# Performance work log

Hardware: AMD Instinct MI355X
Metric: run time of the kernel (lower is better)

The kernel has to match this reference:

```python
import jax, jax.numpy as jnp
from jax import lax
import numpy as np

D_MODEL = 512
D_PROJ = 256
PATCH = 4
NL = 8
D_STATE = 16
D_CONV = 4
EXPAND = 2
D_INNER = EXPAND * D_MODEL          # 1024
DT_RANK = (D_MODEL + 15) // 16      # 32
B = 4
SEQ = 1024
NF = 1
EPS = 1e-5


def setup_inputs() -> dict:
    key = jax.random.key(0)
    ks = jax.random.split(key, 12)
    s = 0.02
    def rn(k, shape):
        return jax.random.normal(k, shape, jnp.float32) * s
    A_init = jnp.log(jnp.arange(1, D_STATE + 1, dtype=jnp.float32))  # (n,)
    return {
        "time_series": jax.random.normal(ks[0], (B, SEQ, NF), jnp.float32),
        "mask": jnp.ones((B, SEQ), jnp.int32),
        "emb_w": rn(ks[1], (D_MODEL, PATCH)),
        "emb_b": jnp.zeros((D_MODEL,), jnp.float32),
        "norm_w": jnp.ones((NL, D_MODEL), jnp.float32),
        "in_w": rn(ks[2], (NL, 2, 2 * D_INNER, D_MODEL)),
        "conv_w": rn(ks[3], (NL, 2, D_INNER, D_CONV)),
        "conv_b": jnp.zeros((NL, 2, D_INNER), jnp.float32),
        "xproj_w": rn(ks[4], (NL, 2, DT_RANK + 2 * D_STATE, D_INNER)),
        "dt_w": rn(ks[5], (NL, 2, D_INNER, DT_RANK)),
        "dt_b": jnp.full((NL, 2, D_INNER), float(np.log(np.expm1(0.01))), jnp.float32),
        "A_log": jnp.broadcast_to(A_init, (NL, 2, D_INNER, D_STATE)) + jnp.zeros((NL, 2, D_INNER, D_STATE), jnp.float32),
        "Dp": jnp.ones((NL, 2, D_INNER), jnp.float32),
        "out_w": rn(ks[6], (NL, 2, D_MODEL, D_INNER)),
        "proj_w": rn(ks[7], (PATCH * D_PROJ, D_MODEL)),
        "proj_b": jnp.zeros((PATCH * D_PROJ,), jnp.float32),
    }


def rmsnorm(x, w):
    return x * lax.rsqrt(jnp.mean(x * x, axis=-1, keepdims=True) + EPS) * w


def mamba(x, in_w, conv_w, conv_b, xproj_w, dt_w, dt_b, A_log, Dp, out_w):
    # x: (B, L, D_MODEL)
    Bsz, L, _ = x.shape
    xz = jnp.einsum('bld,ed->ble', x, in_w)                 # (B,L,2*d_inner)
    u, z = jnp.split(xz, 2, axis=-1)                         # each (B,L,d_inner)
    # depthwise causal conv1d along L
    u_t = jnp.transpose(u, (0, 2, 1))                        # (B,d_inner,L)
    u_pad = jnp.pad(u_t, ((0, 0), (0, 0), (D_CONV - 1, 0)))
    conv = lax.conv_general_dilated(
        u_pad, conv_w[:, None, :], window_strides=(1,), padding='VALID',
        feature_group_count=D_INNER, dimension_numbers=('NCH', 'OIH', 'NCH'))
    u = jax.nn.silu(jnp.transpose(conv + conv_b[None, :, None], (0, 2, 1)))  # (B,L,d_inner)
    x_dbl = jnp.einsum('ble,re->blr', u, xproj_w)            # (B,L,dt_rank+2n)
    dt, Bm, C = jnp.split(x_dbl, [DT_RANK, DT_RANK + D_STATE], axis=-1)
    delta = jax.nn.softplus(jnp.einsum('blr,er->ble', dt, dt_w) + dt_b)  # (B,L,d_inner)
    A = -jnp.exp(A_log)                                      # (d_inner,n)

    def step(h, inp):
        d_t, B_t, C_t, u_t = inp                             # (B,e),(B,n),(B,n),(B,e)
        dA = jnp.exp(d_t[..., None] * A)                     # (B,e,n)
        h = dA * h + (d_t * u_t)[..., None] * B_t[:, None, :]
        y = jnp.einsum('ben,bn->be', h, C_t)
        return h, y

    h0 = jnp.zeros((Bsz, D_INNER, D_STATE), x.dtype)
    xs = (jnp.moveaxis(delta, 1, 0), jnp.moveaxis(Bm, 1, 0),
          jnp.moveaxis(C, 1, 0), jnp.moveaxis(u, 1, 0))
    _, ys = lax.scan(step, h0, xs)                           # ys: (L,B,e)
    y = jnp.moveaxis(ys, 0, 1) + u * Dp
    y = y * jax.nn.silu(z)
    return jnp.einsum('ble,de->bld', y, out_w)               # (B,L,D_MODEL)


def reference(time_series, mask, emb_w, emb_b, norm_w, in_w, conv_w, conv_b,
              xproj_w, dt_w, dt_b, A_log, Dp, out_w, proj_w, proj_b):
    Bsz, S, F_ = time_series.shape
    NP = S // PATCH  # S is a multiple of PATCH
    patches = time_series.reshape(Bsz, NP, PATCH, F_)
    patches = jnp.transpose(patches, (0, 3, 1, 2)).reshape(Bsz, F_ * NP, PATCH)
    x = patches @ emb_w.T + emb_b                            # (B, F*NP, D_MODEL)
    for i in range(NL):
        res = x
        xn = rmsnorm(x, norm_w[i])
        yf = mamba(xn, in_w[i, 0], conv_w[i, 0], conv_b[i, 0], xproj_w[i, 0],
                   dt_w[i, 0], dt_b[i, 0], A_log[i, 0], Dp[i, 0], out_w[i, 0])
        yb = mamba(jnp.flip(xn, axis=1), in_w[i, 1], conv_w[i, 1], conv_b[i, 1],
                   xproj_w[i, 1], dt_w[i, 1], dt_b[i, 1], A_log[i, 1], Dp[i, 1], out_w[i, 1])
        x = yf + jnp.flip(yb, axis=1) + res
    proj = x @ proj_w.T + proj_b                             # (B, F*NP, PATCH*D_PROJ)
    le = proj.reshape(Bsz, F_, NP, PATCH, D_PROJ)
    le = jnp.transpose(le, (0, 2, 3, 1, 4)).reshape(Bsz, NP * PATCH, F_, D_PROJ)
    return le[:, :S]
```

## Files before the change

### kernel.cpp

```cpp
#include <hip/hip_runtime.h>
#include <hip/hip_bf16.h>

#define DM 512
#define DI 1024
#define DSTATE 16
#define DTR 32
#define NLAYER 8
#define BS 4
#define LL 256
#define MT 1024
#define DPROJ 256
#define CL 32
#define NCH (LL/CL)
#define SP 20

typedef unsigned short u16;
typedef __attribute__((ext_vector_type(8))) short short8;
typedef __attribute__((ext_vector_type(4))) float f32x4;

__device__ __forceinline__ float sigmoidf_(float x){ return 1.f/(1.f+__expf(-x)); }

__device__ __forceinline__ u16 f2bf(float f){
  unsigned u = __float_as_uint(f);
  u = (u + 0x7FFF + ((u>>16)&1)) >> 16;
  return (u16)u;
}
__device__ __forceinline__ float bf2f(u16 v){
  return __uint_as_float(((unsigned)v) << 16);
}

template<int CTRL>
__device__ __forceinline__ float dpp_ror_add(float x){
  int y = __builtin_amdgcn_update_dpp(0, __float_as_int(x), CTRL, 0xF, 0xF, false);
  return x + __int_as_float(y);
}
__device__ __forceinline__ float sum16_dpp(float x){
  x = dpp_ror_add<0x128>(x);
  x = dpp_ror_add<0x124>(x);
  x = dpp_ror_add<0x122>(x);
  x = dpp_ror_add<0x121>(x);
  return x;
}

__global__ __launch_bounds__(256) void embed_k(const float* __restrict__ ts,
    const float* __restrict__ ew, const float* __restrict__ eb, float* __restrict__ x){
  int idx = blockIdx.x*256 + threadIdx.x;
  int m = idx >> 9, d = idx & 511;
  int b = m >> 8, np_ = m & 255;
  const float* t0 = ts + b*1024 + np_*4;
  float acc = eb[d];
  #pragma unroll
  for (int p=0;p<4;p++) acc = fmaf(t0[p], ew[d*4+p], acc);
  x[idx] = acc;
}

__global__ __launch_bounds__(256) void wcastall_k(
    const float* __restrict__ w_in, const float* __restrict__ w_out,
    const float* __restrict__ w_xp, const float* __restrict__ w_pj,
    u16* __restrict__ dst){
  int t = blockIdx.x*256 + threadIdx.x;
  long e4 = (long)t*4;
  const float* src; long o;
  if      (e4 < 16777216) { src = w_in;  o = e4; }
  else if (e4 < 25165824) { src = w_out; o = e4 - 16777216; }
  else if (e4 < 26214400) { src = w_xp;  o = e4 - 25165824; }
  else                    { src = w_pj;  o = e4 - 26214400; }
  float4 v = *(const float4*)(src + o);
  ushort4 r; r.x=f2bf(v.x); r.y=f2bf(v.y); r.z=f2bf(v.z); r.w=f2bf(v.w);
  *(ushort4*)(dst + e4) = r;
}

__global__ __launch_bounds__(256) void rmscomb_k(float* __restrict__ x,
    const float* __restrict__ yout,
    const float* __restrict__ nw, u16* __restrict__ xnbf, u16* __restrict__ xnfbf){
  int m = blockIdx.x, t = threadIdx.x;
  int b = m>>8, l = m&255, mf = (b<<8)+(255-l);
  float2 v = *(const float2*)&x[(long)m*DM + t*2];
  if (yout){
    float2 f = *(const float2*)&yout[(long)m*DM + t*2];
    float2 g = *(const float2*)&yout[(long)MT*DM + (long)mf*DM + t*2];
    v.x += f.x + g.x; v.y += f.y + g.y;
    *(float2*)&x[(long)m*DM + t*2] = v;
  }
  float ss = v.x*v.x + v.y*v.y;
  ss += __shfl_down(ss,32); ss += __shfl_down(ss,16); ss += __shfl_down(ss,8);
  ss += __shfl_down(ss,4);  ss += __shfl_down(ss,2);  ss += __shfl_down(ss,1);
  __shared__ float ps[4];
  if ((t&63)==0) ps[t>>6] = ss;
  __syncthreads();
  float tot = ps[0]+ps[1]+ps[2]+ps[3];
  float rs = rsqrtf(tot*(1.f/DM) + 1e-5f);
  ushort2 o; o.x = f2bf(v.x*rs*nw[t*2]); o.y = f2bf(v.y*rs*nw[t*2+1]);
  *(ushort2*)&xnbf [(long)m *DM + t*2] = o;
  *(ushort2*)&xnfbf[(long)mf*DM + t*2] = o;
}

__global__ __launch_bounds__(256) void combcast_k(const float* __restrict__ x,
    const float* __restrict__ yout, u16* __restrict__ xbf){
  int idx = blockIdx.x*256 + threadIdx.x;
  int m = idx >> 7, c4 = idx & 127;
  int b = m>>8, l = m&255, mf = (b<<8)+(255-l);
  float4 r = ((const float4*)x)[idx];
  float4 f = ((const float4*)yout)[idx];
  float4 g = ((const float4*)(yout + (long)MT*DM))[(long)mf*128 + c4];
  ushort4 o;
  o.x = f2bf(r.x + f.x + g.x); o.y = f2bf(r.y + f.y + g.y);
  o.z = f2bf(r.z + f.z + g.z); o.w = f2bf(r.w + f.w + g.w);
  ((ushort4*)xbf)[idx] = o;
}

template<int BM,int BN,int SPLITK,int EPI>
__global__ __launch_bounds__(256) void mfma_nt(
    const u16* __restrict__ A, int lda, long sA,
    const u16* __restrict__ W, int ldw, long sW,
    const float* __restrict__ bias, u16* __restrict__ G,
    float* __restrict__ C, int ldc, long sC,
    int M, int N, int K)
{
  constexpr int WM = BM/2, WN = BN/2;
  constexpr int MI = WM/16, NI = WN/16;
  int z = blockIdx.z;
  int dir = z / SPLITK, kc = z % SPLITK;
  int Klen = K / SPLITK;
  int kbase = kc * Klen;
  A += (long)dir * sA;
  W += (long)dir * sW;
  if (SPLITK > 1) C += (long)z * M * N; else C += (long)dir * sC;
  if (EPI==4) G += (long)dir * (long)MT*DI;

  __shared__ u16 Al[BM*32];
  __shared__ u16 Wl[BN*32];
  int tid = threadIdx.x;
  int lane = tid & 63;
  int wave = tid >> 6;
  int wm0 = (wave>>1)*WM, wn0 = (wave&1)*WN;
  int m0 = blockIdx.y*BM, n0 = blockIdx.x*BN;
  int l16 = lane>>4, l15 = lane&15;

  f32x4 acc[MI][NI] = {};

  for (int k0=0; k0<Klen; k0+=32){
    #pragma unroll
    for (int it=0; it<BM*4/256; ++it){
      int ch = it*256 + tid;
      int row = ch % BM, kk = ch / BM;
      const u16* g = A + (long)(m0+row)*lda + kbase + k0 + kk*8;
      __builtin_amdgcn_global_load_lds(
          (const __attribute__((address_space(1))) void*)g,
          (__attribute__((address_space(3))) void*)(Al + ch*8), 16, 0, 0);
    }
    #pragma unroll
    for (int it=0; it<BN*4/256; ++it){
      int ch = it*256 + tid;
      int row = ch % BN, kk = ch / BN;
      const u16* g = W + (long)(n0+row)*ldw + kbase + k0 + kk*8;
      __builtin_amdgcn_global_load_lds(
          (const __attribute__((address_space(1))) void*)g,
          (__attribute__((address_space(3))) void*)(Wl + ch*8), 16, 0, 0);
    }
    __syncthreads();
    short8 a[MI], b[NI];
    #pragma unroll
    for (int i=0;i<MI;i++)
      a[i] = *(const short8*)&Al[(l16*BM + wm0 + i*16 + l15)*8];
    #pragma unroll
    for (int j=0;j<NI;j++)
      b[j] = *(const short8*)&Wl[(l16*BN + wn0 + j*16 + l15)*8];
    #pragma unroll
    for (int i=0;i<MI;i++)
      #pragma unroll
      for (int j=0;j<NI;j++)
        acc[i][j] = __builtin_amdgcn_mfma_f32_16x16x32_bf16(a[i], b[j], acc[i][j], 0,0,0);
    __syncthreads();
  }
  #pragma unroll
  for (int i=0;i<MI;i++){
    #pragma unroll
    for (int j=0;j<NI;j++){
      #pragma unroll
      for (int r=0;r<4;r++){
        int m = m0 + wm0 + i*16 + l16*4 + r;
        int n = n0 + wn0 + j*16 + l15;
        float v = acc[i][j][r];
        if (EPI==2){
          v += bias[n];
          int bb = m>>8, np_ = m&255, p = n>>8, dp = n&255;
          C[((long)(bb*1024 + np_*4 + p))*256 + dp] = v;
        } else if (EPI==4){
          if (n < 1024) C[(long)m*1024 + n] = v;
          else          G[(long)m*1024 + (n-1024)] = f2bf(v * sigmoidf_(v));
        } else {
          C[(long)m*ldc + n] = v;
        }
      }
    }
  }
}

__global__ __launch_bounds__(256) void xreduce_k(const float* __restrict__ part,
    float* __restrict__ xdbl){
  int idx = blockIdx.x*256 + threadIdx.x;
  int d = idx >> 16, off = idx & 65535;
  float s = 0.f;
  #pragma unroll
  for (int kc=0; kc<8; ++kc) s += part[((d*8+kc)<<16) + off];
  xdbl[idx] = s;
}

__global__ __launch_bounds__(256) void conv_silu_k(const float* __restrict__ xzu,
    const float* __restrict__ cw, const float* __restrict__ cb,
    u16* __restrict__ ubf){
  int idx = blockIdx.x*256 + threadIdx.x;
  int e = idx & (DI-1);
  int grp = idx >> 10;
  int dir = grp >> 8;
  int b   = (grp >> 6) & 3;
  int l0  = (grp & 63) * 4;
  long dm0 = (long)dir*MT + b*LL + l0;
  const float* w = cw + ((long)dir*DI + e)*4;
  float w0=w[0], w1=w[1], w2=w[2], w3=w[3];
  float bias = cb[dir*DI + e];
  const float* src = xzu + dm0*DI + e;
  float vb[7];
  #pragma unroll
  for (int j=0;j<7;j++){
    int l = l0 - 3 + j;
    vb[j] = (l >= 0) ? src[(long)(j-3)*DI] : 0.f;
  }
  #pragma unroll
  for (int j=0;j<4;j++){
    float acc = bias;
    acc = fmaf(w0, vb[j],   acc);
    acc = fmaf(w1, vb[j+1], acc);
    acc = fmaf(w2, vb[j+2], acc);
    acc = fmaf(w3, vb[j+3], acc);
    float v = acc * sigmoidf_(acc);
    ubf[(dm0+j)*DI + e] = f2bf(v);
  }
}

__global__ __launch_bounds__(256) void scan_k(
    const u16* __restrict__ ubf, const u16* __restrict__ gbf,
    const float* __restrict__ xdbl, const float* __restrict__ dtw,
    const float* __restrict__ dtb, const float* __restrict__ A_log,
    const float* __restrict__ Dp, u16* __restrict__ ygbf)
{
  int t = threadIdx.x;
  int n = t & 15, el = t >> 4;
  int ec = blockIdx.x, b = blockIdx.y, dir = blockIdx.z;
  int e0 = ec*16, e = e0 + el;
  float Av = -__expf(A_log[((long)dir*DI + e)*16 + n]);
  float Dv = Dp[dir*DI + e];
  long mbase = (long)dir*MT + b*LL;
  const u16* up_ = ubf + mbase*DI;
  const u16* gp_ = gbf + mbase*DI;
  const float* xd_ = xdbl + mbase*64;
  u16* yp_ = ygbf + mbase*DI;

  float wrow[32];
  {
    const float* wr = dtw + ((long)dir*DI + e0 + n)*32;
    #pragma unroll
    for (int r4=0;r4<8;r4++) *(float4*)&wrow[r4*4] = *(const float4*)&wr[r4*4];
  }
  float dtbv = dtb[dir*DI + e0 + n];

  __shared__ float sdt[2][CL][32];
  __shared__ float sBC[2][CL][32];
  __shared__ float sU [2][CL][SP];
  __shared__ float sD [CL][SP];
  __shared__ float sy [CL][SP];

  float4 xv0, xv1; ushort4 uvv;
  auto load_pre = [&](int c){
    long l0 = (long)c*CL;
    int f0 = t, f1 = t + 256;
    xv0 = *(const float4*)&xd_[(l0 + (f0>>4))*64 + (f0&15)*4];
    xv1 = *(const float4*)&xd_[(l0 + (f1>>4))*64 + (f1&15)*4];
    if (t < 128) uvv = *(const ushort4*)&up_[(l0 + (t>>2))*DI + e0 + (t&3)*4];
  };
  auto write_pre = [&](int buf){
    {
      int row = t>>4, c4 = (t&15)*4;
      if (c4 < 32) *(float4*)&sdt[buf][row][c4] = xv0;
      else         *(float4*)&sBC[buf][row][c4-32] = xv0;
    }
    {
      int f1 = t + 256;
      int row = f1>>4, c4 = (f1&15)*4;
      if (c4 < 32) *(float4*)&sdt[buf][row][c4] = xv1;
      else         *(float4*)&sBC[buf][row][c4-32] = xv1;
    }
    if (t < 128){
      float4 uf;
      uf.x = bf2f(uvv.x); uf.y = bf2f(uvv.y); uf.z = bf2f(uvv.z); uf.w = bf2f(uvv.w);
      *(float4*)&sU[buf][t>>2][(t&3)*4] = uf;
    }
  };

  load_pre(0);
  write_pre(0);
  load_pre(1);
  __syncthreads();

  float h = 0.f;
  for (int c = 0; c < NCH; ++c){
    int cur = c & 1;
    #pragma unroll
    for (int j=0;j<2;j++){
      int l = (t>>4)*2 + j;
      float acc = dtbv;
      #pragma unroll
      for (int r4=0;r4<8;r4++){
        float4 d4 = *(const float4*)&sdt[cur][l][r4*4];
        acc = fmaf(d4.x, wrow[r4*4],   acc);
        acc = fmaf(d4.y, wrow[r4*4+1], acc);
        acc = fmaf(d4.z, wrow[r4*4+2], acc);
        acc = fmaf(d4.w, wrow[r4*4+3], acc);
      }
      acc = fmaxf(acc, 0.f) + __logf(1.f + __expf(-fabsf(acc)));
      sD[l][n] = acc;
    }
    ushort4 gv;
    if (t < 128) gv = *(const ushort4*)&gp_[((long)c*CL + (t>>2))*DI + e0 + (t&3)*4];
    __syncthreads();

    const float* pD  = &sD[0][el];
    const float* pU  = &sU[cur][0][el];
    const float* pBC = &sBC[cur][0][n];
    #pragma unroll
    for (int c8 = 0; c8 < 4; ++c8){
      const float* pD8  = pD  + c8*8*SP;
      const float* pU8  = pU  + c8*8*SP;
      const float* pBC8 = pBC + c8*256;
      #pragma unroll
      for (int l8 = 0; l8 < 8; ++l8){
        float dv = pD8[l8*SP];
        float uv = pU8[l8*SP];
        float Bv = pBC8[l8*32], Cv = pBC8[l8*32 + 16];
        float dA = __expf(dv*Av);
        h = fmaf(dA, h, dv*uv*Bv);
        float yc = sum16_dpp(h*Cv);
        if (n==0) sy[c8*8+l8][el] = yc + uv*Dv;
      }
    }
    __syncthreads();
    if (c+1 < NCH){
      write_pre(cur^1);
      if (c+2 < NCH) load_pre(c+2);
    }
    if (t < 128){
      float4 y4 = *(const float4*)&sy[t>>2][(t&3)*4];
      ushort4 o;
      o.x = f2bf(y4.x * bf2f(gv.x)); o.y = f2bf(y4.y * bf2f(gv.y));
      o.z = f2bf(y4.z * bf2f(gv.z)); o.w = f2bf(y4.w * bf2f(gv.w));
      *(ushort4*)&yp_[((long)c*CL + (t>>2))*DI + e0 + (t&3)*4] = o;
    }
    __syncthreads();
  }
}

extern "C" void kernel_launch(void* const* d_in, const int* in_sizes, int n_in,
                              void* d_out, int out_size, void* d_ws, size_t ws_size,
                              hipStream_t stream){
  const float* ts   = (const float*)d_in[0];
  const float* ew   = (const float*)d_in[2];
  const float* eb   = (const float*)d_in[3];
  const float* nw   = (const float*)d_in[4];
  const float* inw  = (const float*)d_in[5];
  const float* cw   = (const float*)d_in[6];
  const float* cb   = (const float*)d_in[7];
  const float* xpw  = (const float*)d_in[8];
  const float* dtw  = (const float*)d_in[9];
  const float* dtb  = (const float*)d_in[10];
  const float* alog = (const float*)d_in[11];
  const float* dpp  = (const float*)d_in[12];
  const float* outw = (const float*)d_in[13];
  const float* pw   = (const float*)d_in[14];
  const float* pb   = (const float*)d_in[15];
  float* out = (float*)d_out;

  float* ws   = (float*)d_ws;
  float* x    = ws;
  float* xzu  = ws + 524288;
  float* xdbl = ws + 2621440;
  float* yout = ws + 2752512;
  float* xpart= ws + 3801088;
  u16* ub     = (u16*)(ws + 4849664);
  u16* xn_bf  = ub;
  u16* u_bf   = ub + 1048576;
  u16* g_bf   = ub + 3145728;
  u16* yg_bf  = ub + 5242880;
  u16* x_bf   = ub + 7340032;
  u16* wb     = ub + 7864320;
  u16* wb_in  = wb;
  u16* wb_out = wb + 16777216;
  u16* wb_xp  = wb + 25165824;
  u16* wb_pj  = wb + 26214400;

  dim3 blk(256);

  embed_k<<<MT*DM/256, blk, 0, stream>>>(ts, ew, eb, x);
  wcastall_k<<<26112, blk, 0, stream>>>(inw, outw, xpw, pw, wb);

  for (int i=0;i<NLAYER;i++){
    rmscomb_k<<<MT, blk, 0, stream>>>(x, i ? yout : nullptr, nw + i*DM,
        xn_bf, xn_bf + MT*DM);
    mfma_nt<64,128,1,4><<<dim3(16,16,2), blk, 0, stream>>>(
        xn_bf, DM, (long)MT*DM, wb_in + (long)i*2097152, DM, 1048576,
        nullptr, g_bf, xzu, 1024, (long)MT*1024, MT, 2048, DM);
    conv_silu_k<<<2048, blk, 0, stream>>>(xzu, cw + (long)i*2*DI*4, cb + i*2*DI, u_bf);
    mfma_nt<64,64,8,0><<<dim3(1,16,16), blk, 0, stream>>>(
        u_bf, DI, (long)MT*DI, wb_xp + (long)i*131072, DI, 65536,
        nullptr, nullptr, xpart, 64, 0, MT, 64, DI);
    xreduce_k<<<512, blk, 0, stream>>>(xpart, xdbl);
    scan_k<<<dim3(64, BS, 2), blk, 0, stream>>>(u_bf, g_bf, xdbl,
        dtw + (long)i*2*DI*DTR, dtb + (long)i*2*DI,
        alog + (long)i*2*DI*16, dpp + i*2*DI, yg_bf);
    mfma_nt<64,64,1,0><<<dim3(8,16,2), blk, 0, stream>>>(
        yg_bf, DI, (long)MT*DI, wb_out + (long)i*1048576, DI, 524288,
        nullptr, nullptr, yout, DM, (long)MT*DM, MT, DM, DI);
  }
  combcast_k<<<MT*DM/4/256, blk, 0, stream>>>(x, yout, x_bf);
  mfma_nt<64,64,1,2><<<dim3(16,16,1), blk, 0, stream>>>(
      x_bf, DM, 0, wb_pj, DM, 0, pb, nullptr, out, 1024, 0, MT, 1024, DM);
}
```

Baseline: 766.4 us.

## Transpose scan shared-memory layout for vector loads and remap blocks across XCDs

```diff
diff --git a/kernel.cpp b/kernel.cpp
--- a/kernel.cpp
+++ b/kernel.cpp
@@ -12,7 +12,6 @@
 #define DPROJ 256
 #define CL 32
 #define NCH (LL/CL)
-#define SP 20
 
 typedef unsigned short u16;
 typedef __attribute__((ext_vector_type(8))) short short8;
@@ -247,7 +246,12 @@
 {
   int t = threadIdx.x;
   int n = t & 15, el = t >> 4;
-  int ec = blockIdx.x, b = blockIdx.y, dir = blockIdx.z;
+  int id = blockIdx.x + 64*blockIdx.y + 256*blockIdx.z;
+  int xcd = id & 7, slot = id >> 3;
+  int ec = xcd*8 + (slot & 7);
+  int bd = slot >> 3;
+  int b = bd & 3, dir = bd >> 2;
+
   int e0 = ec*16, e = e0 + el;
   float Av = -__expf(A_log[((long)dir*DI + e)*16 + n]);
   float Dv = Dp[dir*DI + e];
@@ -265,11 +269,10 @@
   }
   float dtbv = dtb[dir*DI + e0 + n];
 
-  __shared__ float sdt[2][CL][32];
-  __shared__ float sBC[2][CL][32];
-  __shared__ float sU [2][CL][SP];
-  __shared__ float sD [CL][SP];
-  __shared__ float sy [CL][SP];
+  __shared__ float sDU[2][16][68];
+  __shared__ float sBC[2][16][68];
+  __shared__ float sdt[2][32][36];
+  __shared__ float sy [32][20];
 
   float4 xv0, xv1; ushort4 uvv;
   auto load_pre = [&](int c){
@@ -280,21 +283,29 @@
     if (t < 128) uvv = *(const ushort4*)&up_[(l0 + (t>>2))*DI + e0 + (t&3)*4];
   };
   auto write_pre = [&](int buf){
-    {
-      int row = t>>4, c4 = (t&15)*4;
-      if (c4 < 32) *(float4*)&sdt[buf][row][c4] = xv0;
-      else         *(float4*)&sBC[buf][row][c4-32] = xv0;
-    }
-    {
-      int f1 = t + 256;
-      int row = f1>>4, c4 = (f1&15)*4;
-      if (c4 < 32) *(float4*)&sdt[buf][row][c4] = xv1;
-      else         *(float4*)&sBC[buf][row][c4-32] = xv1;
+    #pragma unroll
+    for (int h_=0; h_<2; ++h_){
+      float4 xv = h_ ? xv1 : xv0;
+      int f = t + h_*256;
+      int row = f>>4, c4 = (f&15)*4;
+      if (c4 < 32){
+        *(float4*)&sdt[buf][row][c4] = xv;
+      } else if (c4 < 48){
+        int nb = c4 - 32;
+        sBC[buf][nb  ][row*2] = xv.x; sBC[buf][nb+1][row*2] = xv.y;
+        sBC[buf][nb+2][row*2] = xv.z; sBC[buf][nb+3][row*2] = xv.w;
+      } else {
+        int nb = c4 - 48;
+        sBC[buf][nb  ][row*2+1] = xv.x; sBC[buf][nb+1][row*2+1] = xv.y;
+        sBC[buf][nb+2][row*2+1] = xv.z; sBC[buf][nb+3][row*2+1] = xv.w;
+      }
     }
     if (t < 128){
-      float4 uf;
-      uf.x = bf2f(uvv.x); uf.y = bf2f(uvv.y); uf.z = bf2f(uvv.z); uf.w = bf2f(uvv.w);
-      *(float4*)&sU[buf][t>>2][(t&3)*4] = uf;
+      int l = t>>2, e4 = (t&3)*4;
+      sDU[buf][e4  ][l*2+1] = bf2f(uvv.x);
+      sDU[buf][e4+1][l*2+1] = bf2f(uvv.y);
+      sDU[buf][e4+2][l*2+1] = bf2f(uvv.z);
+      sDU[buf][e4+3][l*2+1] = bf2f(uvv.w);
     }
   };
 
@@ -304,11 +315,12 @@
   __syncthreads();
 
   float h = 0.f;
+  int lp = t >> 4;
   for (int c = 0; c < NCH; ++c){
     int cur = c & 1;
     #pragma unroll
     for (int j=0;j<2;j++){
-      int l = (t>>4)*2 + j;
+      int l = lp + j*16;
       float acc = dtbv;
       #pragma unroll
       for (int r4=0;r4<8;r4++){
@@ -319,29 +331,29 @@
         acc = fmaf(d4.w, wrow[r4*4+3], acc);
       }
       acc = fmaxf(acc, 0.f) + __logf(1.f + __expf(-fabsf(acc)));
-      sD[l][n] = acc;
+      sDU[cur][n][l*2] = acc;
     }
     ushort4 gv;
     if (t < 128) gv = *(const ushort4*)&gp_[((long)c*CL + (t>>2))*DI + e0 + (t&3)*4];
     __syncthreads();
 
-    const float* pD  = &sD[0][el];
-    const float* pU  = &sU[cur][0][el];
-    const float* pBC = &sBC[cur][0][n];
-    #pragma unroll
-    for (int c8 = 0; c8 < 4; ++c8){
-      const float* pD8  = pD  + c8*8*SP;
-      const float* pU8  = pU  + c8*8*SP;
-      const float* pBC8 = pBC + c8*256;
-      #pragma unroll
-      for (int l8 = 0; l8 < 8; ++l8){
-        float dv = pD8[l8*SP];
-        float uv = pU8[l8*SP];
-        float Bv = pBC8[l8*32], Cv = pBC8[l8*32 + 16];
-        float dA = __expf(dv*Av);
-        h = fmaf(dA, h, dv*uv*Bv);
-        float yc = sum16_dpp(h*Cv);
-        if (n==0) sy[c8*8+l8][el] = yc + uv*Dv;
+    const float* pDU = &sDU[cur][el][0];
+    const float* pBC = &sBC[cur][n][0];
+    #pragma unroll
+    for (int l2 = 0; l2 < 16; ++l2){
+      float4 du = *(const float4*)&pDU[l2*4];
+      float4 bc = *(const float4*)&pBC[l2*4];
+      {
+        float dA = __expf(du.x*Av);
+        h = fmaf(dA, h, du.x*du.y*bc.x);
+        float yc = sum16_dpp(h*bc.y);
+        if (n==0) sy[2*l2][el] = yc + du.y*Dv;
+      }
+      {
+        float dA = __expf(du.z*Av);
+        h = fmaf(dA, h, du.z*du.w*bc.z);
+        float yc = sum16_dpp(h*bc.w);
+        if (n==0) sy[2*l2+1][el] = yc + du.w*Dv;
       }
     }
     __syncthreads();
```

Measured after the change: 750.2 us. -2.1%, faster.

## Restructure selective scan into single-wave blocks with XCD-aware channel mapping

Applied to the files above, without the earlier changes.

```diff
diff --git a/kernel.cpp b/kernel.cpp
--- a/kernel.cpp
+++ b/kernel.cpp
@@ -10,11 +10,9 @@
 #define LL 256
 #define MT 1024
 #define DPROJ 256
-#define CL 32
-#define NCH (LL/CL)
-#define SP 20
 
 typedef unsigned short u16;
+typedef unsigned int u32;
 typedef __attribute__((ext_vector_type(8))) short short8;
 typedef __attribute__((ext_vector_type(4))) float f32x4;
 
@@ -239,122 +237,122 @@
   }
 }
 
-__global__ __launch_bounds__(256) void scan_k(
+__global__ __launch_bounds__(64) void scan_k(
     const u16* __restrict__ ubf, const u16* __restrict__ gbf,
     const float* __restrict__ xdbl, const float* __restrict__ dtw,
     const float* __restrict__ dtb, const float* __restrict__ A_log,
     const float* __restrict__ Dp, u16* __restrict__ ygbf)
 {
   int t = threadIdx.x;
-  int n = t & 15, el = t >> 4;
-  int ec = blockIdx.x, b = blockIdx.y, dir = blockIdx.z;
-  int e0 = ec*16, e = e0 + el;
-  float Av = -__expf(A_log[((long)dir*DI + e)*16 + n]);
-  float Dv = Dp[dir*DI + e];
+  int n = t & 15, g = t >> 4;
+  int id = blockIdx.x + 256*blockIdx.y + 1024*blockIdx.z;
+  int xcd = id & 7, s = id >> 3;
+  int ecb = xcd*32 + (s & 31);
+  int rest = s >> 5;
+  int b = rest & 3, dir = rest >> 2;
+  int e0 = ecb*4;
+
   long mbase = (long)dir*MT + b*LL;
-  const u16* up_ = ubf + mbase*DI;
-  const u16* gp_ = gbf + mbase*DI;
+  const u16* up_ = ubf + mbase*DI + e0;
+  const u16* gp_ = gbf + mbase*DI + e0;
   const float* xd_ = xdbl + mbase*64;
-  u16* yp_ = ygbf + mbase*DI;
+  u16* yp_ = ygbf + mbase*DI + e0;
+
+  float Av = -__expf(A_log[((long)dir*DI + e0 + g)*16 + n]);
+  float Dv = Dp[dir*DI + e0 + g];
 
   float wrow[32];
   {
-    const float* wr = dtw + ((long)dir*DI + e0 + n)*32;
+    const float* wr = dtw + ((long)dir*DI + e0 + g)*32;
     #pragma unroll
     for (int r4=0;r4<8;r4++) *(float4*)&wrow[r4*4] = *(const float4*)&wr[r4*4];
   }
-  float dtbv = dtb[dir*DI + e0 + n];
-
-  __shared__ float sdt[2][CL][32];
-  __shared__ float sBC[2][CL][32];
-  __shared__ float sU [2][CL][SP];
-  __shared__ float sD [CL][SP];
-  __shared__ float sy [CL][SP];
-
-  float4 xv0, xv1; ushort4 uvv;
-  auto load_pre = [&](int c){
-    long l0 = (long)c*CL;
-    int f0 = t, f1 = t + 256;
-    xv0 = *(const float4*)&xd_[(l0 + (f0>>4))*64 + (f0&15)*4];
-    xv1 = *(const float4*)&xd_[(l0 + (f1>>4))*64 + (f1&15)*4];
-    if (t < 128) uvv = *(const ushort4*)&up_[(l0 + (t>>2))*DI + e0 + (t&3)*4];
+  float dtbv = dtb[dir*DI + e0 + g];
+
+  __shared__ u32 sDU[32][4][2];
+  __shared__ u32 sBC[32][20];
+  __shared__ float sy[32][4];
+
+  ushort4 ru, rg;
+  float4 rb0, rb1, rc0, rc1;
+  int brow = t >> 1, bseg = t & 1;
+
+  auto loadrg = [&](int c){
+    int l0 = c*32;
+    if (t < 32){
+      ru = *(const ushort4*)&up_[(long)(l0 + t)*DI];
+      rg = *(const ushort4*)&gp_[(long)(l0 + t)*DI];
+    }
+    const float* src = &xd_[(long)(l0 + brow)*64 + 32 + bseg*8];
+    rb0 = *(const float4*)&src[0];
+    rb1 = *(const float4*)&src[4];
+    rc0 = *(const float4*)&src[16];
+    rc1 = *(const float4*)&src[20];
   };
-  auto write_pre = [&](int buf){
+
+  loadrg(0);
+  float h = 0.f;
+
+  for (int c = 0; c < 8; ++c){
+    int l0 = c*32;
+    if (t < 32){
+      sDU[t][0][1] = ru.x; sDU[t][1][1] = ru.y;
+      sDU[t][2][1] = ru.z; sDU[t][3][1] = ru.w;
+    }
     {
-      int row = t>>4, c4 = (t&15)*4;
-      if (c4 < 32) *(float4*)&sdt[buf][row][c4] = xv0;
-      else         *(float4*)&sBC[buf][row][c4-32] = xv0;
-    }
-    {
-      int f1 = t + 256;
-      int row = f1>>4, c4 = (f1&15)*4;
-      if (c4 < 32) *(float4*)&sdt[buf][row][c4] = xv1;
-      else         *(float4*)&sBC[buf][row][c4-32] = xv1;
-    }
-    if (t < 128){
-      float4 uf;
-      uf.x = bf2f(uvv.x); uf.y = bf2f(uvv.y); uf.z = bf2f(uvv.z); uf.w = bf2f(uvv.w);
-      *(float4*)&sU[buf][t>>2][(t&3)*4] = uf;
-    }
-  };
-
-  load_pre(0);
-  write_pre(0);
-  load_pre(1);
-  __syncthreads();
-
-  float h = 0.f;
-  for (int c = 0; c < NCH; ++c){
-    int cur = c & 1;
+      uint4 p0, p1;
+      p0.x = (u32)f2bf(rb0.x) | ((u32)f2bf(rc0.x)<<16);
+      p0.y = (u32)f2bf(rb0.y) | ((u32)f2bf(rc0.y)<<16);
+      p0.z = (u32)f2bf(rb0.z) | ((u32)f2bf(rc0.z)<<16);
+      p0.w = (u32)f2bf(rb0.w) | ((u32)f2bf(rc0.w)<<16);
+      p1.x = (u32)f2bf(rb1.x) | ((u32)f2bf(rc1.x)<<16);
+      p1.y = (u32)f2bf(rb1.y) | ((u32)f2bf(rc1.y)<<16);
+      p1.z = (u32)f2bf(rb1.z) | ((u32)f2bf(rc1.z)<<16);
+      p1.w = (u32)f2bf(rb1.w) | ((u32)f2bf(rc1.w)<<16);
+      *(uint4*)&sBC[brow][bseg*8]     = p0;
+      *(uint4*)&sBC[brow][bseg*8 + 4] = p1;
+    }
     #pragma unroll
     for (int j=0;j<2;j++){
-      int l = (t>>4)*2 + j;
+      int l = n + j*16;
+      const float* row = &xd_[(long)(l0 + l)*64];
       float acc = dtbv;
       #pragma unroll
       for (int r4=0;r4<8;r4++){
-        float4 d4 = *(const float4*)&sdt[cur][l][r4*4];
+        float4 d4 = *(const float4*)&row[r4*4];
         acc = fmaf(d4.x, wrow[r4*4],   acc);
         acc = fmaf(d4.y, wrow[r4*4+1], acc);
         acc = fmaf(d4.z, wrow[r4*4+2], acc);
         acc = fmaf(d4.w, wrow[r4*4+3], acc);
       }
       acc = fmaxf(acc, 0.f) + __logf(1.f + __expf(-fabsf(acc)));
-      sD[l][n] = acc;
-    }
-    ushort4 gv;
-    if (t < 128) gv = *(const ushort4*)&gp_[((long)c*CL + (t>>2))*DI + e0 + (t&3)*4];
+      sDU[l][g][0] = __float_as_uint(acc);
+    }
+    ushort4 gcur = rg;
     __syncthreads();
-
-    const float* pD  = &sD[0][el];
-    const float* pU  = &sU[cur][0][el];
-    const float* pBC = &sBC[cur][0][n];
-    #pragma unroll
-    for (int c8 = 0; c8 < 4; ++c8){
-      const float* pD8  = pD  + c8*8*SP;
-      const float* pU8  = pU  + c8*8*SP;
-      const float* pBC8 = pBC + c8*256;
-      #pragma unroll
-      for (int l8 = 0; l8 < 8; ++l8){
-        float dv = pD8[l8*SP];
-        float uv = pU8[l8*SP];
-        float Bv = pBC8[l8*32], Cv = pBC8[l8*32 + 16];
-        float dA = __expf(dv*Av);
-        h = fmaf(dA, h, dv*uv*Bv);
-        float yc = sum16_dpp(h*Cv);
-        if (n==0) sy[c8*8+l8][el] = yc + uv*Dv;
-      }
-    }
-    __syncthreads();
-    if (c+1 < NCH){
-      write_pre(cur^1);
-      if (c+2 < NCH) load_pre(c+2);
-    }
-    if (t < 128){
-      float4 y4 = *(const float4*)&sy[t>>2][(t&3)*4];
+    if (c < 7) loadrg(c+1);
+
+    #pragma unroll 8
+    for (int l = 0; l < 32; ++l){
+      uint2 du = *(const uint2*)&sDU[l][g][0];
+      float dv = __uint_as_float(du.x);
+      float uv = bf2f((u16)du.y);
+      u32 bc = sBC[l][n];
+      float Bv = bf2f((u16)(bc & 0xffff));
+      float Cv = bf2f((u16)(bc >> 16));
+      float dA = __expf(dv*Av);
+      h = fmaf(dA, h, dv*uv*Bv);
+      float yc = sum16_dpp(h*Cv);
+      if (n==0) sy[l][g] = yc + uv*Dv;
+    }
+    __builtin_amdgcn_wave_barrier();
+
+    if (t < 32){
+      float4 y4 = *(const float4*)&sy[t][0];
       ushort4 o;
-      o.x = f2bf(y4.x * bf2f(gv.x)); o.y = f2bf(y4.y * bf2f(gv.y));
-      o.z = f2bf(y4.z * bf2f(gv.z)); o.w = f2bf(y4.w * bf2f(gv.w));
-      *(ushort4*)&yp_[((long)c*CL + (t>>2))*DI + e0 + (t&3)*4] = o;
+      o.x = f2bf(y4.x * bf2f(gcur.x)); o.y = f2bf(y4.y * bf2f(gcur.y));
+      o.z = f2bf(y4.z * bf2f(gcur.z)); o.w = f2bf(y4.w * bf2f(gcur.w));
+      *(ushort4*)&yp_[(long)(l0 + t)*DI] = o;
     }
     __syncthreads();
   }
@@ -414,7 +412,7 @@
         u_bf, DI, (long)MT*DI, wb_xp + (long)i*131072, DI, 65536,
         nullptr, nullptr, xpart, 64, 0, MT, 64, DI);
     xreduce_k<<<512, blk, 0, stream>>>(xpart, xdbl);
-    scan_k<<<dim3(64, BS, 2), blk, 0, stream>>>(u_bf, g_bf, xdbl,
+    scan_k<<<dim3(256, BS, 2), dim3(64), 0, stream>>>(u_bf, g_bf, xdbl,
         dtw + (long)i*2*DI*DTR, dtb + (long)i*2*DI,
         alog + (long)i*2*DI*16, dpp + i*2*DI, yg_bf);
     mfma_nt<64,64,1,0><<<dim3(8,16,2), blk, 0, stream>>>(
```

Measured after the change: 870.3 us. +13.5%, slower.
